# Optimization experiments

Measured on AMD Instinct MI355X. Metric: run time of the kernel, lower is better.

The kernel has to match this reference:

```python
import jax, jax.numpy as jnp
import numpy as np

DT = 0.001
TAU_SYN = 0.01
TAU_MEM = 0.005
THRESHOLD = 1.0
ALPHA = float(np.exp(-DT / TAU_SYN))  # syn decay
BETA = float(np.exp(-DT / TAU_MEM))   # mem decay

BATCH, IN_SIZE, OUT_SIZE = 4096, 2048, 2048


@jax.custom_vjp
def spike(x):
    # Heaviside forward with sigmoid-derivative surrogate gradient
    return (x > 0).astype(x.dtype)

def _spike_fwd(x):
    return spike(x), x

def _spike_bwd(x, g):
    s = jax.nn.sigmoid(x)
    return (g * s * (1.0 - s),)

spike.defvjp(_spike_fwd, _spike_bwd)


def setup_inputs() -> dict:
    key = jax.random.key(0)
    k1, k2, k3, k4, k5 = jax.random.split(key, 5)
    inputs = jax.random.normal(k1, (BATCH, IN_SIZE), dtype=jnp.float32)
    I = jax.random.normal(k2, (BATCH, OUT_SIZE), dtype=jnp.float32)
    V = jax.random.normal(k3, (BATCH, OUT_SIZE), dtype=jnp.float32)
    Z = jnp.zeros((BATCH, OUT_SIZE), dtype=jnp.float32)
    # initialize_weights_: ndim<=2 -> normal init
    fwd_w = jax.random.normal(k4, (IN_SIZE, OUT_SIZE), dtype=jnp.float32)
    rec_w = jax.random.normal(k5, (OUT_SIZE, OUT_SIZE), dtype=jnp.float32)
    return {"inputs": inputs, "I": I, "V": V, "Z": Z,
            "fwd_w": fwd_w, "rec_w": rec_w}


def reference(inputs, I, V, Z, fwd_w, rec_w):
    # LIFLayer.forward_Erme, single timestep
    input_current = jnp.matmul(inputs, fwd_w)          # [B, O]
    rec_current = jnp.matmul(Z, rec_w)                 # [B, O]
    is_active = 1.0 - jax.lax.stop_gradient(Z)
    next_I = ALPHA * I + input_current + rec_current
    next_V = (BETA * V + next_I) * is_active
    next_Z = spike(next_V - THRESHOLD)
    return next_Z, next_I, next_V
```

## Files before the change

### kernel.cpp

```cpp
#include <hip/hip_runtime.h>
#include <cstdint>
#include <cstddef>

typedef __bf16 bf16_t;
typedef __bf16 bf16x4 __attribute__((ext_vector_type(4)));
typedef __bf16 bf16x8 __attribute__((ext_vector_type(8)));
typedef float f32x4 __attribute__((ext_vector_type(4)));

#define M_DIM 4096
#define K_DIM 2048
#define N_DIM 2048

#define BM 128
#define BN 128
#define BK 64
#define KT (K_DIM / BK)
#define A_EL (BM * BK)
#define B_EL (BN * BK)
#define PER_BUF (A_EL + B_EL)
#define B_OFF A_EL

#define ZCAP 64

#define MFMA16(a, b, c) \
  __builtin_amdgcn_mfma_f32_16x16x32_bf16((a), (b), (c), 0, 0, 0)

__device__ __forceinline__ void gload_lds16(const bf16_t* g, bf16_t* l) {
  __builtin_amdgcn_global_load_lds(
      (const __attribute__((address_space(1))) void*)g,
      (__attribute__((address_space(3))) void*)l, 16, 0, 0);
}

__global__ __launch_bounds__(256) void convert_a(
    const float* __restrict__ inputs, bf16_t* __restrict__ abf) {
  const int g = blockIdx.x * 256 + threadIdx.x;
  const size_t base = (size_t)g * 8;
  const float4 v0 = *reinterpret_cast<const float4*>(inputs + base);
  const float4 v1 = *reinterpret_cast<const float4*>(inputs + base + 4);
  bf16x8 o;
  o[0] = (bf16_t)v0.x; o[1] = (bf16_t)v0.y;
  o[2] = (bf16_t)v0.z; o[3] = (bf16_t)v0.w;
  o[4] = (bf16_t)v1.x; o[5] = (bf16_t)v1.y;
  o[6] = (bf16_t)v1.z; o[7] = (bf16_t)v1.w;
  *reinterpret_cast<bf16x8*>(abf + base) = o;
}

__global__ __launch_bounds__(256) void transpose_w(
    const float* __restrict__ src, bf16_t* __restrict__ dst) {
  __shared__ float tile[64][65];
  const int t = threadIdx.x;
  const int k0 = blockIdx.y * 64;
  const int n0 = blockIdx.x * 64;
#pragma unroll
  for (int p = 0; p < 4; ++p) {
    const int r = p * 16 + (t >> 4);
    const int c = (t & 15) * 4;
    const float4 v = *reinterpret_cast<const float4*>(
        &src[(size_t)(k0 + r) * N_DIM + n0 + c]);
    tile[r][c + 0] = v.x;
    tile[r][c + 1] = v.y;
    tile[r][c + 2] = v.z;
    tile[r][c + 3] = v.w;
  }
  __syncthreads();
#pragma unroll
  for (int p = 0; p < 4; ++p) {
    const int n = p * 16 + (t >> 4);
    const int c = (t & 15) * 4;
    bf16x4 o;
    o[0] = (bf16_t)tile[c + 0][n];
    o[1] = (bf16_t)tile[c + 1][n];
    o[2] = (bf16_t)tile[c + 2][n];
    o[3] = (bf16_t)tile[c + 3][n];
    *reinterpret_cast<bf16x4*>(&dst[(size_t)(n0 + n) * K_DIM + k0 + c]) = o;
  }
}

__global__ __launch_bounds__(256) void scan_z(
    const float* __restrict__ Z, int* __restrict__ zcnt,
    int* __restrict__ zidx, float* __restrict__ zval) {
  const int row = blockIdx.x * 4 + (threadIdx.x >> 6);
  const int lane = threadIdx.x & 63;
  const float* zr = Z + (size_t)row * N_DIM;
  int local = 0;
#pragma unroll
  for (int c = 0; c < 32; c += 4) {
    const f32x4 v = *reinterpret_cast<const f32x4*>(zr + lane * 32 + c);
#pragma unroll
    for (int e = 0; e < 4; ++e) local += (v[e] != 0.0f) ? 1 : 0;
  }
  int pre = local;
#pragma unroll
  for (int d = 1; d < 64; d <<= 1) {
    const int up = __shfl_up(pre, d, 64);
    if (lane >= d) pre += up;
  }
  const int total = __shfl(pre, 63, 64);
  if (lane == 0) zcnt[row] = total;
  if (total > 0 && total <= ZCAP) {
    int wpos = pre - local;
    int* zi = zidx + (size_t)row * ZCAP;
    float* zv = zval + (size_t)row * ZCAP;
    for (int c = lane * 32; c < lane * 32 + 32; ++c) {
      const float v = zr[c];
      if (v != 0.0f) {
        zi[wpos] = c;
        zv[wpos] = v;
        ++wpos;
      }
    }
  }
}

__global__ __launch_bounds__(256, 2) void lif_gemm_db(
    const bf16_t* __restrict__ A, const bf16_t* __restrict__ W,
    const float* __restrict__ recw,
    const int* __restrict__ zcnt, const int* __restrict__ zidx,
    const float* __restrict__ zval,
    const float* __restrict__ Iin, const float* __restrict__ Vin,
    const float* __restrict__ Zin,
    float* __restrict__ outZ, float* __restrict__ outI,
    float* __restrict__ outV) {
  __shared__ __align__(16) bf16_t lds[2 * PER_BUF];

  const int tid = threadIdx.x;
  const int lane = tid & 63;
  const int wave = tid >> 6;
  const int wm = wave >> 1;
  const int wn = wave & 1;
  const int l15 = lane & 15;
  const int l4 = lane >> 4;

  const int bid = blockIdx.x;
  const int swz = (bid & 7) * 64 + (bid >> 3);
  const int m0 = (swz >> 4) * BM;
  const int n0 = (swz & 15) * BN;

  const int lr = lane >> 3;
  const int sg = (lane & 7) ^ lr;
  const bf16_t* aSrc[4];
  const bf16_t* bSrc[4];
  int aDst[4], bDst[4];
#pragma unroll
  for (int i = 0; i < 4; ++i) {
    const int r = wave * 32 + i * 8 + lr;
    aSrc[i] = A + (size_t)(m0 + r) * K_DIM + sg * 8;
    aDst[i] = r * BK + (lane & 7) * 8;
    bSrc[i] = W + (size_t)(n0 + r) * K_DIM + sg * 8;
    bDst[i] = B_OFF + r * BK + (lane & 7) * 8;
  }

  int aBase[2], bBase[2];
#pragma unroll
  for (int ks = 0; ks < 2; ++ks) {
    const int phys = (l4 + ks * 4) ^ (l15 & 7);
    aBase[ks] = (wm * 64 + l15) * BK + phys * 8;
    bBase[ks] = B_OFF + (wn * 64 + l15) * BK + phys * 8;
  }

  f32x4 acc[4][4];
#pragma unroll
  for (int i = 0; i < 4; ++i)
#pragma unroll
    for (int j = 0; j < 4; ++j)
#pragma unroll
      for (int e = 0; e < 4; ++e) acc[i][j][e] = 0.0f;

#pragma unroll
  for (int i = 0; i < 4; ++i) {
    gload_lds16(aSrc[i], lds + aDst[i]);
    gload_lds16(bSrc[i], lds + bDst[i]);
  }
#pragma unroll
  for (int i = 0; i < 4; ++i) {
    gload_lds16(aSrc[i] + BK, lds + PER_BUF + aDst[i]);
    gload_lds16(bSrc[i] + BK, lds + PER_BUF + bDst[i]);
  }
  asm volatile("s_waitcnt vmcnt(8)" ::: "memory");
  __builtin_amdgcn_sched_barrier(0);
  __builtin_amdgcn_s_barrier();
  __builtin_amdgcn_sched_barrier(0);

  for (int t = 0; t < KT; ++t) {
    const bf16_t* bufC = lds + (t & 1) * PER_BUF;
    bf16_t* bufS = lds + (t & 1) * PER_BUF;

    bf16x8 af[4][2], bfr[4][2];
#pragma unroll
    for (int mi = 0; mi < 4; ++mi)
#pragma unroll
      for (int ks = 0; ks < 2; ++ks)
        af[mi][ks] =
            *reinterpret_cast<const bf16x8*>(bufC + aBase[ks] + mi * 1024);
#pragma unroll
    for (int ni = 0; ni < 4; ++ni)
#pragma unroll
      for (int ks = 0; ks < 2; ++ks)
        bfr[ni][ks] =
            *reinterpret_cast<const bf16x8*>(bufC + bBase[ks] + ni * 1024);
    asm volatile("s_waitcnt lgkmcnt(0)" ::: "memory");
    __builtin_amdgcn_sched_barrier(0);
    __builtin_amdgcn_s_barrier();
    __builtin_amdgcn_sched_barrier(0);

    if (t + 2 < KT) {
      const int kt = (t + 2) * BK;
#pragma unroll
      for (int i = 0; i < 4; ++i) {
        gload_lds16(aSrc[i] + kt, bufS + aDst[i]);
        gload_lds16(bSrc[i] + kt, bufS + bDst[i]);
      }
    }

    __builtin_amdgcn_s_setprio(1);
#pragma unroll
    for (int mi = 0; mi < 4; ++mi)
#pragma unroll
      for (int ni = 0; ni < 4; ++ni) {
        acc[mi][ni] = MFMA16(af[mi][0], bfr[ni][0], acc[mi][ni]);
        acc[mi][ni] = MFMA16(af[mi][1], bfr[ni][1], acc[mi][ni]);
      }
    __builtin_amdgcn_s_setprio(0);
    __builtin_amdgcn_sched_barrier(0);

    if (t + 2 < KT) {
      asm volatile("s_waitcnt vmcnt(8)" ::: "memory");
    } else if (t + 1 < KT) {
      asm volatile("s_waitcnt vmcnt(0)" ::: "memory");
    }
    __builtin_amdgcn_sched_barrier(0);
    __builtin_amdgcn_s_barrier();
    __builtin_amdgcn_sched_barrier(0);
  }

  const float alpha = 0.90483741803595957f;
  const float beta = 0.81873075307798182f;
  float* swp = reinterpret_cast<float*>(lds) + wave * (16 * 66);
  const int er = lane >> 2;
  const int ec = (lane & 3) * 4;

#pragma unroll
  for (int mi = 0; mi < 4; ++mi) {
#pragma unroll
    for (int ni = 0; ni < 4; ++ni)
#pragma unroll
      for (int j = 0; j < 4; ++j)
        swp[(l4 * 4 + j) * 66 + ni * 16 + l15] = acc[mi][ni][j];

    const int row = m0 + wm * 64 + mi * 16 + er;
    const int colb = n0 + wn * 64 + ec;
    const int cnt = zcnt[row];

    f32x4 rec4[4], gate4[4];
#pragma unroll
    for (int cc = 0; cc < 4; ++cc)
#pragma unroll
      for (int e = 0; e < 4; ++e) {
        rec4[cc][e] = 0.0f;
        gate4[cc][e] = 1.0f;
      }
    if (cnt > 0) {
      if (cnt <= ZCAP) {
        const int* zi = zidx + (size_t)row * ZCAP;
        const float* zv = zval + (size_t)row * ZCAP;
        for (int s = 0; s < cnt; ++s) {
          const int o = zi[s];
          const float v = zv[s];
          const float* wr = recw + (size_t)o * N_DIM + colb;
#pragma unroll
          for (int cc = 0; cc < 4; ++cc) {
            const f32x4 wv = *reinterpret_cast<const f32x4*>(wr + cc * 16);
#pragma unroll
            for (int e = 0; e < 4; ++e) {
              rec4[cc][e] += v * wv[e];
              gate4[cc][e] = (o == colb + cc * 16 + e) ? (1.0f - v)
                                                       : gate4[cc][e];
            }
          }
        }
      } else {
        const float* zr = Zin + (size_t)row * N_DIM;
        for (int o = 0; o < N_DIM; ++o) {
          const float v = zr[o];
          if (v != 0.0f) {
            const float* wr = recw + (size_t)o * N_DIM + colb;
#pragma unroll
            for (int cc = 0; cc < 4; ++cc) {
              const f32x4 wv = *reinterpret_cast<const f32x4*>(wr + cc * 16);
#pragma unroll
              for (int e = 0; e < 4; ++e) {
                rec4[cc][e] += v * wv[e];
                gate4[cc][e] = (o == colb + cc * 16 + e) ? (1.0f - v)
                                                         : gate4[cc][e];
              }
            }
          }
        }
      }
    }

    const size_t gb = (size_t)row * N_DIM + colb;
#pragma unroll
    for (int cc = 0; cc < 4; ++cc) {
      const f32x4 av =
          *reinterpret_cast<const f32x4*>(swp + er * 66 + ec + cc * 16);
      const f32x4 iv = *reinterpret_cast<const f32x4*>(Iin + gb + cc * 16);
      const f32x4 vv = *reinterpret_cast<const f32x4*>(Vin + gb + cc * 16);
      f32x4 nI, nV, nZ;
#pragma unroll
      for (int e = 0; e < 4; ++e) {
        nI[e] = alpha * iv[e] + av[e] + rec4[cc][e];
        nV[e] = (beta * vv[e] + nI[e]) * gate4[cc][e];
        nZ[e] = (nV[e] > 1.0f) ? 1.0f : 0.0f;
      }
      *reinterpret_cast<f32x4*>(outI + gb + cc * 16) = nI;
      *reinterpret_cast<f32x4*>(outV + gb + cc * 16) = nV;
      *reinterpret_cast<f32x4*>(outZ + gb + cc * 16) = nZ;
    }
  }
}

extern "C" void kernel_launch(void* const* d_in, const int* in_sizes, int n_in,
                              void* d_out, int out_size, void* d_ws,
                              size_t ws_size, hipStream_t stream) {
  const float* inputs = (const float*)d_in[0];
  const float* I = (const float*)d_in[1];
  const float* V = (const float*)d_in[2];
  const float* Z = (const float*)d_in[3];
  const float* fwd_w = (const float*)d_in[4];
  const float* rec_w = (const float*)d_in[5];

  float* outZ = (float*)d_out;
  float* outI = outZ + (size_t)M_DIM * N_DIM;
  float* outV = outI + (size_t)M_DIM * N_DIM;

  bf16_t* abf = (bf16_t*)d_ws;
  bf16_t* wT = (bf16_t*)((char*)d_ws + (size_t)M_DIM * K_DIM * 2);
  char* p = (char*)d_ws + (size_t)M_DIM * K_DIM * 2 + (size_t)N_DIM * K_DIM * 2;
  int* zcnt = (int*)p;
  int* zidx = (int*)(p + M_DIM * 4);
  float* zval = (float*)(p + M_DIM * 4 + (size_t)M_DIM * ZCAP * 4);

  hipLaunchKernelGGL(convert_a, dim3((M_DIM * K_DIM) / (256 * 8)), dim3(256),
                     0, stream, inputs, abf);
  hipLaunchKernelGGL(transpose_w, dim3(N_DIM / 64, K_DIM / 64), dim3(256), 0,
                     stream, fwd_w, wT);
  hipLaunchKernelGGL(scan_z, dim3(M_DIM / 4), dim3(256), 0, stream, Z, zcnt,
                     zidx, zval);
  hipLaunchKernelGGL(lif_gemm_db, dim3((M_DIM / BM) * (N_DIM / BN)),
                     dim3(256), 0, stream, abf, wT, rec_w, zcnt, zidx, zval, I,
                     V, Z, outZ, outI, outV);
}
```

Measured before the change: 88.74 us.

## Fuse prepass kernels and use triple-buffered BK=32 GEMM pipeline

Merges the three preprocessing kernels (input conversion, weight transpose, Z scan) into one launch that picks its role from the block index. In the GEMM it halves the K tile to 32, switches from two to three LDS buffers with a new XOR swizzle, and issues the prefetch for tile t+2 before reading the current tile, which removes one barrier per iteration. The intent is fewer kernel launches and less barrier stall per iteration, at the cost of twice as many loop iterations, each with a smaller MFMA batch.

```diff
diff --git a/kernel.cpp b/kernel.cpp
--- a/kernel.cpp
+++ b/kernel.cpp
@@ -13,7 +13,7 @@
 
 #define BM 128
 #define BN 128
-#define BK 64
+#define BK 32
 #define KT (K_DIM / BK)
 #define A_EL (BM * BK)
 #define B_EL (BN * BK)
@@ -31,88 +31,88 @@
       (__attribute__((address_space(3))) void*)l, 16, 0, 0);
 }
 
-__global__ __launch_bounds__(256) void convert_a(
-    const float* __restrict__ inputs, bf16_t* __restrict__ abf) {
-  const int g = blockIdx.x * 256 + threadIdx.x;
-  const size_t base = (size_t)g * 8;
-  const float4 v0 = *reinterpret_cast<const float4*>(inputs + base);
-  const float4 v1 = *reinterpret_cast<const float4*>(inputs + base + 4);
-  bf16x8 o;
-  o[0] = (bf16_t)v0.x; o[1] = (bf16_t)v0.y;
-  o[2] = (bf16_t)v0.z; o[3] = (bf16_t)v0.w;
-  o[4] = (bf16_t)v1.x; o[5] = (bf16_t)v1.y;
-  o[6] = (bf16_t)v1.z; o[7] = (bf16_t)v1.w;
-  *reinterpret_cast<bf16x8*>(abf + base) = o;
+__global__ __launch_bounds__(256) void prepass_all(
+    const float* __restrict__ inputs, const float* __restrict__ fwd_w,
+    const float* __restrict__ Z, bf16_t* __restrict__ abf,
+    bf16_t* __restrict__ wT, int* __restrict__ zcnt, int* __restrict__ zidx,
+    float* __restrict__ zval) {
+  __shared__ float tile[64][65];
+  const int b = blockIdx.x;
+  const int t = threadIdx.x;
+
+  if (b < 4096) {
+    const size_t base = ((size_t)b * 256 + t) * 8;
+    const float4 v0 = *reinterpret_cast<const float4*>(inputs + base);
+    const float4 v1 = *reinterpret_cast<const float4*>(inputs + base + 4);
+    bf16x8 o;
+    o[0] = (bf16_t)v0.x; o[1] = (bf16_t)v0.y;
+    o[2] = (bf16_t)v0.z; o[3] = (bf16_t)v0.w;
+    o[4] = (bf16_t)v1.x; o[5] = (bf16_t)v1.y;
+    o[6] = (bf16_t)v1.z; o[7] = (bf16_t)v1.w;
+    *reinterpret_cast<bf16x8*>(abf + base) = o;
+  } else if (b < 5120) {
+    const int bb = b - 4096;
+    const int n0 = (bb & 31) * 64;
+    const int k0 = (bb >> 5) * 64;
+#pragma unroll
+    for (int p = 0; p < 4; ++p) {
+      const int r = p * 16 + (t >> 4);
+      const int c = (t & 15) * 4;
+      const float4 v = *reinterpret_cast<const float4*>(
+          &fwd_w[(size_t)(k0 + r) * N_DIM + n0 + c]);
+      tile[r][c + 0] = v.x;
+      tile[r][c + 1] = v.y;
+      tile[r][c + 2] = v.z;
+      tile[r][c + 3] = v.w;
+    }
+    __syncthreads();
+#pragma unroll
+    for (int p = 0; p < 4; ++p) {
+      const int n = p * 16 + (t >> 4);
+      const int c = (t & 15) * 4;
+      bf16x4 o;
+      o[0] = (bf16_t)tile[c + 0][n];
+      o[1] = (bf16_t)tile[c + 1][n];
+      o[2] = (bf16_t)tile[c + 2][n];
+      o[3] = (bf16_t)tile[c + 3][n];
+      *reinterpret_cast<bf16x4*>(&wT[(size_t)(n0 + n) * K_DIM + k0 + c]) = o;
+    }
+  } else {
+    const int row = (b - 5120) * 4 + (t >> 6);
+    const int lane = t & 63;
+    const float* zr = Z + (size_t)row * N_DIM;
+    int local = 0;
+#pragma unroll
+    for (int c = 0; c < 32; c += 4) {
+      const f32x4 v = *reinterpret_cast<const f32x4*>(zr + lane * 32 + c);
+#pragma unroll
+      for (int e = 0; e < 4; ++e) local += (v[e] != 0.0f) ? 1 : 0;
+    }
+    int pre = local;
+#pragma unroll
+    for (int d = 1; d < 64; d <<= 1) {
+      const int up = __shfl_up(pre, d, 64);
+      if (lane >= d) pre += up;
+    }
+    const int total = __shfl(pre, 63, 64);
+    if (lane == 0) zcnt[row] = total;
+    if (total > 0 && total <= ZCAP) {
+      int wpos = pre - local;
+      int* zi = zidx + (size_t)row * ZCAP;
+      float* zv = zval + (size_t)row * ZCAP;
+      for (int c = lane * 32; c < lane * 32 + 32; ++c) {
+        const float v = zr[c];
+        if (v != 0.0f) {
+          zi[wpos] = c;
+          zv[wpos] = v;
+          ++wpos;
+        }
+      }
+    }
+  }
 }
 
-__global__ __launch_bounds__(256) void transpose_w(
-    const float* __restrict__ src, bf16_t* __restrict__ dst) {
-  __shared__ float tile[64][65];
-  const int t = threadIdx.x;
-  const int k0 = blockIdx.y * 64;
-  const int n0 = blockIdx.x * 64;
-#pragma unroll
-  for (int p = 0; p < 4; ++p) {
-    const int r = p * 16 + (t >> 4);
-    const int c = (t & 15) * 4;
-    const float4 v = *reinterpret_cast<const float4*>(
-        &src[(size_t)(k0 + r) * N_DIM + n0 + c]);
-    tile[r][c + 0] = v.x;
-    tile[r][c + 1] = v.y;
-    tile[r][c + 2] = v.z;
-    tile[r][c + 3] = v.w;
-  }
-  __syncthreads();
-#pragma unroll
-  for (int p = 0; p < 4; ++p) {
-    const int n = p * 16 + (t >> 4);
-    const int c = (t & 15) * 4;
-    bf16x4 o;
-    o[0] = (bf16_t)tile[c + 0][n];
-    o[1] = (bf16_t)tile[c + 1][n];
-    o[2] = (bf16_t)tile[c + 2][n];
-    o[3] = (bf16_t)tile[c + 3][n];
-    *reinterpret_cast<bf16x4*>(&dst[(size_t)(n0 + n) * K_DIM + k0 + c]) = o;
-  }
-}
-
-__global__ __launch_bounds__(256) void scan_z(
-    const float* __restrict__ Z, int* __restrict__ zcnt,
-    int* __restrict__ zidx, float* __restrict__ zval) {
-  const int row = blockIdx.x * 4 + (threadIdx.x >> 6);
-  const int lane = threadIdx.x & 63;
-  const float* zr = Z + (size_t)row * N_DIM;
-  int local = 0;
-#pragma unroll
-  for (int c = 0; c < 32; c += 4) {
-    const f32x4 v = *reinterpret_cast<const f32x4*>(zr + lane * 32 + c);
-#pragma unroll
-    for (int e = 0; e < 4; ++e) local += (v[e] != 0.0f) ? 1 : 0;
-  }
-  int pre = local;
-#pragma unroll
-  for (int d = 1; d < 64; d <<= 1) {
-    const int up = __shfl_up(pre, d, 64);
-    if (lane >= d) pre += up;
-  }
-  const int total = __shfl(pre, 63, 64);
-  if (lane == 0) zcnt[row] = total;
-  if (total > 0 && total <= ZCAP) {
-    int wpos = pre - local;
-    int* zi = zidx + (size_t)row * ZCAP;
-    float* zv = zval + (size_t)row * ZCAP;
-    for (int c = lane * 32; c < lane * 32 + 32; ++c) {
-      const float v = zr[c];
-      if (v != 0.0f) {
-        zi[wpos] = c;
-        zv[wpos] = v;
-        ++wpos;
-      }
-    }
-  }
-}
-
-__global__ __launch_bounds__(256, 2) void lif_gemm_db(
+__global__ __launch_bounds__(256, 2) void lif_gemm_3b(
     const bf16_t* __restrict__ A, const bf16_t* __restrict__ W,
     const float* __restrict__ recw,
     const int* __restrict__ zcnt, const int* __restrict__ zidx,
@@ -121,7 +121,7 @@
     const float* __restrict__ Zin,
     float* __restrict__ outZ, float* __restrict__ outI,
     float* __restrict__ outV) {
-  __shared__ __align__(16) bf16_t lds[2 * PER_BUF];
+  __shared__ __align__(16) bf16_t lds[3 * PER_BUF];
 
   const int tid = threadIdx.x;
   const int lane = tid & 63;
@@ -136,27 +136,24 @@
   const int m0 = (swz >> 4) * BM;
   const int n0 = (swz & 15) * BN;
 
-  const int lr = lane >> 3;
-  const int sg = (lane & 7) ^ lr;
-  const bf16_t* aSrc[4];
-  const bf16_t* bSrc[4];
-  int aDst[4], bDst[4];
-#pragma unroll
-  for (int i = 0; i < 4; ++i) {
-    const int r = wave * 32 + i * 8 + lr;
+  const int lr = lane >> 2;
+  const int sl = lane & 3;
+  const bf16_t* aSrc[2];
+  const bf16_t* bSrc[2];
+  int aDst[2], bDst[2];
+#pragma unroll
+  for (int i = 0; i < 2; ++i) {
+    const int r = wave * 32 + i * 16 + lr;
+    const int sg = sl ^ ((r >> 1) & 3);
     aSrc[i] = A + (size_t)(m0 + r) * K_DIM + sg * 8;
-    aDst[i] = r * BK + (lane & 7) * 8;
+    aDst[i] = r * BK + sl * 8;
     bSrc[i] = W + (size_t)(n0 + r) * K_DIM + sg * 8;
-    bDst[i] = B_OFF + r * BK + (lane & 7) * 8;
-  }
-
-  int aBase[2], bBase[2];
-#pragma unroll
-  for (int ks = 0; ks < 2; ++ks) {
-    const int phys = (l4 + ks * 4) ^ (l15 & 7);
-    aBase[ks] = (wm * 64 + l15) * BK + phys * 8;
-    bBase[ks] = B_OFF + (wn * 64 + l15) * BK + phys * 8;
-  }
+    bDst[i] = B_OFF + r * BK + sl * 8;
+  }
+
+  const int aphys = l4 ^ ((l15 >> 1) & 3);
+  const int aBase = (wm * 64 + l15) * BK + aphys * 8;
+  const int bBase = B_OFF + (wn * 64 + l15) * BK + aphys * 8;
 
   f32x4 acc[4][4];
 #pragma unroll
@@ -167,70 +164,64 @@
       for (int e = 0; e < 4; ++e) acc[i][j][e] = 0.0f;
 
 #pragma unroll
-  for (int i = 0; i < 4; ++i) {
+  for (int i = 0; i < 2; ++i) {
     gload_lds16(aSrc[i], lds + aDst[i]);
     gload_lds16(bSrc[i], lds + bDst[i]);
   }
 #pragma unroll
-  for (int i = 0; i < 4; ++i) {
+  for (int i = 0; i < 2; ++i) {
     gload_lds16(aSrc[i] + BK, lds + PER_BUF + aDst[i]);
     gload_lds16(bSrc[i] + BK, lds + PER_BUF + bDst[i]);
   }
-  asm volatile("s_waitcnt vmcnt(8)" ::: "memory");
+  asm volatile("s_waitcnt vmcnt(4)" ::: "memory");
   __builtin_amdgcn_sched_barrier(0);
   __builtin_amdgcn_s_barrier();
   __builtin_amdgcn_sched_barrier(0);
 
+  int bt = 0;
   for (int t = 0; t < KT; ++t) {
-    const bf16_t* bufC = lds + (t & 1) * PER_BUF;
-    bf16_t* bufS = lds + (t & 1) * PER_BUF;
-
-    bf16x8 af[4][2], bfr[4][2];
+    bf16_t* bufC = lds + bt * PER_BUF;
+    const int sIdx = (bt == 0) ? 2 : bt - 1;
+    bf16_t* bufS = lds + sIdx * PER_BUF;
+
+    if (t + 2 < KT) {
+      const int kt = (t + 2) * BK;
+#pragma unroll
+      for (int i = 0; i < 2; ++i) {
+        gload_lds16(aSrc[i] + kt, bufS + aDst[i]);
+        gload_lds16(bSrc[i] + kt, bufS + bDst[i]);
+      }
+    }
+
+    bf16x8 af[4], bfr[4];
 #pragma unroll
     for (int mi = 0; mi < 4; ++mi)
-#pragma unroll
-      for (int ks = 0; ks < 2; ++ks)
-        af[mi][ks] =
-            *reinterpret_cast<const bf16x8*>(bufC + aBase[ks] + mi * 1024);
+      af[mi] = *reinterpret_cast<const bf16x8*>(bufC + aBase + mi * 512);
 #pragma unroll
     for (int ni = 0; ni < 4; ++ni)
-#pragma unroll
-      for (int ks = 0; ks < 2; ++ks)
-        bfr[ni][ks] =
-            *reinterpret_cast<const bf16x8*>(bufC + bBase[ks] + ni * 1024);
+      bfr[ni] = *reinterpret_cast<const bf16x8*>(bufC + bBase + ni * 512);
     asm volatile("s_waitcnt lgkmcnt(0)" ::: "memory");
+    __builtin_amdgcn_sched_barrier(0);
+
+    __builtin_amdgcn_s_setprio(1);
+#pragma unroll
+    for (int mi = 0; mi < 4; ++mi)
+#pragma unroll
+      for (int ni = 0; ni < 4; ++ni)
+        acc[mi][ni] = MFMA16(af[mi], bfr[ni], acc[mi][ni]);
+    __builtin_amdgcn_s_setprio(0);
+    __builtin_amdgcn_sched_barrier(0);
+
+    if (t + 2 < KT) {
+      asm volatile("s_waitcnt vmcnt(4)" ::: "memory");
+    } else if (t + 1 < KT) {
+      asm volatile("s_waitcnt vmcnt(0)" ::: "memory");
+    }
     __builtin_amdgcn_sched_barrier(0);
     __builtin_amdgcn_s_barrier();
     __builtin_amdgcn_sched_barrier(0);
 
-    if (t + 2 < KT) {
-      const int kt = (t + 2) * BK;
-#pragma unroll
-      for (int i = 0; i < 4; ++i) {
-        gload_lds16(aSrc[i] + kt, bufS + aDst[i]);
-        gload_lds16(bSrc[i] + kt, bufS + bDst[i]);
-      }
-    }
-
-    __builtin_amdgcn_s_setprio(1);
-#pragma unroll
-    for (int mi = 0; mi < 4; ++mi)
-#pragma unroll
-      for (int ni = 0; ni < 4; ++ni) {
-        acc[mi][ni] = MFMA16(af[mi][0], bfr[ni][0], acc[mi][ni]);
-        acc[mi][ni] = MFMA16(af[mi][1], bfr[ni][1], acc[mi][ni]);
-      }
-    __builtin_amdgcn_s_setprio(0);
-    __builtin_amdgcn_sched_barrier(0);
-
-    if (t + 2 < KT) {
-      asm volatile("s_waitcnt vmcnt(8)" ::: "memory");
-    } else if (t + 1 < KT) {
-      asm volatile("s_waitcnt vmcnt(0)" ::: "memory");
-    }
-    __builtin_amdgcn_sched_barrier(0);
-    __builtin_amdgcn_s_barrier();
-    __builtin_amdgcn_sched_barrier(0);
+    bt = (bt == 2) ? 0 : bt + 1;
   }
 
   const float alpha = 0.90483741803595957f;
@@ -341,13 +332,9 @@
   int* zidx = (int*)(p + M_DIM * 4);
   float* zval = (float*)(p + M_DIM * 4 + (size_t)M_DIM * ZCAP * 4);
 
-  hipLaunchKernelGGL(convert_a, dim3((M_DIM * K_DIM) / (256 * 8)), dim3(256),
-                     0, stream, inputs, abf);
-  hipLaunchKernelGGL(transpose_w, dim3(N_DIM / 64, K_DIM / 64), dim3(256), 0,
-                     stream, fwd_w, wT);
-  hipLaunchKernelGGL(scan_z, dim3(M_DIM / 4), dim3(256), 0, stream, Z, zcnt,
-                     zidx, zval);
-  hipLaunchKernelGGL(lif_gemm_db, dim3((M_DIM / BM) * (N_DIM / BN)),
+  hipLaunchKernelGGL(prepass_all, dim3(6144), dim3(256), 0, stream, inputs,
+                     fwd_w, Z, abf, wT, zcnt, zidx, zval);
+  hipLaunchKernelGGL(lif_gemm_3b, dim3((M_DIM / BM) * (N_DIM / BN)),
                      dim3(256), 0, stream, abf, wT, rec_w, zcnt, zidx, zval, I,
                      V, Z, outZ, outI, outV);
 }
```

Result: slower. 93.41 us (+5.3%).
